# Kernel tuning notes

Measured on AMD Instinct MI355X. Metric: run time of the kernel, lower is better.

Reference implementation:

```python
import jax, jax.numpy as jnp
import numpy as np

P = 2  # sampling ratio: keep top ceil(M/p) measurements


def setup_inputs() -> dict:
    key = jax.random.key(0)
    k1, k2, k3 = jax.random.split(key, 3)
    B, H, W, C = 8, 1024, 1024, 3
    Y = jax.random.normal(k1, (B, H, W, C), dtype=jnp.float32)
    # build()-time Z0 components: abs ~ N(0.5, 0.1), angle ~ N(0, 0.5*sqrt(pi))
    Z0_abs = 0.5 + 0.1 * jax.random.normal(k2, (1, 1, H, W), dtype=jnp.float32)
    Z0_angle = (0.5 * np.pi ** 0.5) * jax.random.normal(k3, (1, 1, H, W), dtype=jnp.float32)
    return {"Y": Y, "Z0_abs": Z0_abs, "Z0_angle": Z0_angle}


def _make_Z0(Z0_abs, Z0_angle):
    # Z0 = |Z0| * exp(i*angle), Frobenius-normalized over spatial axes (2,3)
    Z0 = Z0_abs.astype(jnp.complex64) * jnp.exp(1j * Z0_angle.astype(jnp.complex64))
    fro = jnp.sqrt(jnp.sum(jnp.abs(Z0) ** 2, axis=(2, 3), keepdims=True)).astype(jnp.complex64)
    return Z0 / fro


def reference(Y, Z0_abs, Z0_angle):
    B, H, W, C = Y.shape
    M = H * W * C
    R = int(np.ceil(M / P))
    # transpose NHWC -> NCHW, scale by original S[2] (= W)
    Y_S = jnp.transpose(Y.astype(jnp.float32), (0, 3, 1, 2)) / jnp.float32(W)
    y_s = Y_S.reshape(B, M)
    # threshold = R-th largest value per batch (== descending-sorted index R-1)
    thr = jax.lax.top_k(y_s, R)[0][:, -1]  # [B]
    Ytr = (Y_S >= thr[:, None, None, None]).astype(jnp.float32)  # [B,C,H,W]
    Z0 = _make_Z0(Z0_abs, Z0_angle)
    return Ytr, Z0
```

## Files before the change

kernel.cpp:

```cpp
#include <hip/hip_runtime.h>
#include <math.h>

#define BATCH 8
#define HH 1024
#define WW 1024
#define CC 3
#define MTOT (HH*WW*CC)
#define RSEL 1572864u

#define WCAP 131072u
#define LCAP 1024u
#define P1B  2048
#define QPT  4

#define U_HI 0xBC800000u
#define U_LO 0x437FFFFFu

#define WS_WCNT_OFF  0u
#define WS_CHI_OFF   512u
#define WS_NPART_OFF 1024u
#define WS_THR_OFF   2048u
#define WS_FB_OFF    2112u
#define WS_WU_OFF    4096u
#define WS_WP_OFF    4198400u

#define NCOPY 3
#define HSTRIDE 4097

__device__ __forceinline__ unsigned int fmap(float x) {
    unsigned int b = __float_as_uint(x);
    return (b & 0x80000000u) ? ~b : (b | 0x80000000u);
}

__device__ __forceinline__ void thresh_row_quad(const float* __restrict__ Yb,
                                                float* __restrict__ outb,
                                                int h, int w4, unsigned int tu) {
    const float4* src = (const float4*)(Yb + ((size_t)h * WW + (size_t)w4 * 4) * CC);
    float4 a0 = src[0], a1 = src[1], a2 = src[2];
    float4 r0, r1, r2;
    r0.x = (fmap(a0.x) >= tu) ? 1.f : 0.f;
    r0.y = (fmap(a0.w) >= tu) ? 1.f : 0.f;
    r0.z = (fmap(a1.z) >= tu) ? 1.f : 0.f;
    r0.w = (fmap(a2.y) >= tu) ? 1.f : 0.f;
    r1.x = (fmap(a0.y) >= tu) ? 1.f : 0.f;
    r1.y = (fmap(a1.x) >= tu) ? 1.f : 0.f;
    r1.z = (fmap(a1.w) >= tu) ? 1.f : 0.f;
    r1.w = (fmap(a2.z) >= tu) ? 1.f : 0.f;
    r2.x = (fmap(a0.z) >= tu) ? 1.f : 0.f;
    r2.y = (fmap(a1.y) >= tu) ? 1.f : 0.f;
    r2.z = (fmap(a2.x) >= tu) ? 1.f : 0.f;
    r2.w = (fmap(a2.w) >= tu) ? 1.f : 0.f;
    size_t base = (size_t)h * WW;
    ((float4*)(outb + base))[w4]                        = r0;
    ((float4*)(outb + base + (size_t)HH * WW))[w4]      = r1;
    ((float4*)(outb + base + (size_t)2 * HH * WW))[w4]  = r2;
}

__global__ void __launch_bounds__(256, 4) pass1_kernel(
                             const float* __restrict__ Y,
                             const float* __restrict__ zabs,
                             float* __restrict__ out,
                             unsigned int* __restrict__ wu,
                             unsigned int* __restrict__ wpos,
                             unsigned int* __restrict__ wcnt,
                             unsigned int* __restrict__ chib,
                             float* __restrict__ npart) {
    const int tid = threadIdx.x;

    if (blockIdx.x >= P1B) {
        const int bx = blockIdx.x - P1B;
        float s = 0.f;
        const int n4z = HH * WW / 4;
        for (int i = bx * 256 + tid; i < n4z; i += 256 * 256) {
            float4 v = ((const float4*)zabs)[i];
            s += v.x * v.x + v.y * v.y + v.z * v.z + v.w * v.w;
        }
        for (int d = 32; d > 0; d >>= 1) s += __shfl_down(s, d);
        __shared__ float ls[4];
        if ((tid & 63) == 0) ls[tid >> 6] = s;
        __syncthreads();
        if (tid == 0) npart[bx] = ls[0] + ls[1] + ls[2] + ls[3];
        return;
    }

    __shared__ unsigned int lu[LCAP];
    __shared__ unsigned int lp[LCAP];
    __shared__ unsigned int lcnt;
    __shared__ unsigned int red[4];
    __shared__ unsigned int gbase_s;
    if (tid == 0) lcnt = 0u;
    __syncthreads();

    const int blk = blockIdx.x;
    const int b = blk >> 8;
    const int p0 = (blk & 255) * 1024 + tid;
    const float* Yb = Y + (size_t)b * MTOT;
    float* outb = out + (size_t)b * MTOT;
    float4* o4 = (float4*)outb;

    float4 A0[QPT], A1[QPT], A2[QPT];
#pragma unroll
    for (int it = 0; it < QPT; it++) {
        int p = p0 + it * 256;
        const float4* src = (const float4*)(Yb + (size_t)p * 12);
        A0[it] = src[0]; A1[it] = src[1]; A2[it] = src[2];
    }
    __builtin_amdgcn_sched_barrier(0);

    unsigned int hcnt = 0u;
    unsigned long long wmask = 0ull;

#pragma unroll
    for (int it = 0; it < QPT; it++) {
        const int p = p0 + it * 256;
        float4 a0 = A0[it], a1 = A1[it], a2 = A2[it];
        float4 r0, r1, r2;

#define CLS(val, dst, j) do { \
        unsigned int u = fmap(val); \
        bool hi = (u >= U_HI); \
        dst = hi ? 1.f : 0.f; \
        hcnt += hi ? 1u : 0u; \
        if (!hi && u >= U_LO) wmask |= (1ull << (it * 12 + (j))); \
    } while (0)

        CLS(a0.x, r0.x, 0); CLS(a0.w, r0.y, 1); CLS(a1.z, r0.z, 2); CLS(a2.y, r0.w, 3);
        CLS(a0.y, r1.x, 4); CLS(a1.x, r1.y, 5); CLS(a1.w, r1.z, 6); CLS(a2.z, r1.w, 7);
        CLS(a0.z, r2.x, 8); CLS(a1.y, r2.y, 9); CLS(a2.x, r2.z, 10); CLS(a2.w, r2.w, 11);
#undef CLS

        o4[p]           = r0;
        o4[262144 + p]  = r1;
        o4[524288 + p]  = r2;
    }

    if (wmask) {
        unsigned int nw = (unsigned int)__popcll(wmask);
        unsigned int base = atomicAdd(&lcnt, nw);
#pragma unroll
        for (int it = 0; it < QPT; it++) {
            const int p = p0 + it * 256;
            const unsigned int rb = (unsigned int)(4 * p);
            float4 a0 = A0[it], a1 = A1[it], a2 = A2[it];
#define EMIT(val, ch, k, j) do { \
            if (wmask & (1ull << (it * 12 + (j)))) { \
                if (base < LCAP) { lu[base] = fmap(val); lp[base] = (unsigned int)((ch) * HH * WW) + rb + (k); } \
                base++; \
            } \
        } while (0)
            EMIT(a0.x, 0, 0, 0); EMIT(a0.w, 0, 1, 1); EMIT(a1.z, 0, 2, 2); EMIT(a2.y, 0, 3, 3);
            EMIT(a0.y, 1, 0, 4); EMIT(a1.x, 1, 1, 5); EMIT(a1.w, 1, 2, 6); EMIT(a2.z, 1, 3, 7);
            EMIT(a0.z, 2, 0, 8); EMIT(a1.y, 2, 1, 9); EMIT(a2.x, 2, 2, 10); EMIT(a2.w, 2, 3, 11);
#undef EMIT
        }
    }

    __syncthreads();
    unsigned int n = lcnt;
    unsigned int nc = (n > LCAP) ? LCAP : n;
    if (tid == 0) {
        unsigned int add = (n > LCAP) ? (WCAP + 1u) : n;
        gbase_s = atomicAdd(&wcnt[b * 16], add);
    }
    for (int d = 32; d > 0; d >>= 1) hcnt += __shfl_down(hcnt, d);
    if ((tid & 63) == 0) red[tid >> 6] = hcnt;
    __syncthreads();
    if (tid == 0) atomicAdd(&chib[b * 16], red[0] + red[1] + red[2] + red[3]);

    unsigned int gbase = gbase_s;
    unsigned int* wub = wu + (size_t)b * WCAP;
    unsigned int* wpb = wpos + (size_t)b * WCAP;
    for (unsigned int j = tid; j < nc; j += 256u) {
        unsigned int q = gbase + j;
        if (q < WCAP) { wub[q] = lu[j]; wpb[q] = lp[j]; }
    }
}

__global__ void __launch_bounds__(1024) refine_kernel(
        const float* __restrict__ Y,
        const unsigned int* __restrict__ wu,
        const unsigned int* __restrict__ wcnt,
        const unsigned int* __restrict__ chib,
        const float* __restrict__ npart,
        unsigned int* __restrict__ thr,
        unsigned int* __restrict__ fbflag,
        const float* __restrict__ zabs,
        const float* __restrict__ zang,
        float* __restrict__ outz, int interleaved) {
    const int tid = threadIdx.x;

    if (blockIdx.x >= 8) {
        const int z = blockIdx.x - 8;
        __shared__ float ls[4];
        float s = (tid < 256) ? npart[tid] : 0.f;
        for (int d = 32; d > 0; d >>= 1) s += __shfl_down(s, d);
        if (tid < 256 && (tid & 63) == 0) ls[tid >> 6] = s;
        __syncthreads();
        float inv = 1.0f / sqrtf(ls[0] + ls[1] + ls[2] + ls[3]);
        int i = z * 1024 + tid;
        float2 a = ((const float2*)zabs)[i];
        float2 g = ((const float2*)zang)[i];
        float s0, c0, s1, c1;
        __sincosf(g.x, &s0, &c0);
        __sincosf(g.y, &s1, &c1);
        if (interleaved) {
            float4 o;
            o.x = a.x * c0 * inv; o.y = a.x * s0 * inv;
            o.z = a.y * c1 * inv; o.w = a.y * s1 * inv;
            ((float4*)outz)[i] = o;
        } else {
            float2 o;
            o.x = a.x * c0 * inv; o.y = a.y * c1 * inv;
            ((float2*)outz)[i] = o;
        }
        return;
    }

    __shared__ unsigned int hist[NCOPY * HSTRIDE];
    __shared__ unsigned int waveSums[16];
    __shared__ unsigned int selBin, selBase;
    const int b = blockIdx.x;
    const int lane = tid & 63, wid = tid >> 6;
    const int hc = (wid % NCOPY) * HSTRIDE;

    const unsigned int wc = wcnt[b * 16];
    const unsigned int Ch = chib[b * 16];
    const int fb = (wc > WCAP) || (Ch >= RSEL) || (Ch + wc < RSEL);
    unsigned int target = fb ? RSEL : (RSEL - Ch);
    const unsigned int wcg = (wc > WCAP) ? WCAP : wc;
    const unsigned int* wp = wu + (size_t)b * WCAP;
    const float* Yb = Y + (size_t)b * MTOT;

    unsigned int d1 = 0, d2 = 0;

    for (int level = 0; level < 3; level++) {
        const int nb  = (level < 2) ? 4096 : 256;
        const int bpt = (level < 2) ? 4 : 1;
        for (int i = tid; i < NCOPY * HSTRIDE; i += 1024) hist[i] = 0u;
        if (tid == 0) { selBin = 0u; selBase = 0u; }
        __syncthreads();

#define HISTO(u) do { \
            if (level == 0) atomicAdd(&hist[hc + ((u) >> 20)], 1u); \
            else if (level == 1) { if (((u) >> 20) == d1) atomicAdd(&hist[hc + (((u) >> 8) & 0xFFFu)], 1u); } \
            else { if (((u) >> 8) == ((d1 << 12) | d2)) atomicAdd(&hist[hc + ((u) & 0xFFu)], 1u); } \
        } while (0)

        if (fb) {
            for (unsigned int i = tid; i < (unsigned int)MTOT; i += 1024u) {
                unsigned int u = fmap(Yb[i]);
                HISTO(u);
            }
        } else {
            for (unsigned int i = tid; i < wcg; i += 1024u) {
                unsigned int u = wp[i];
                HISTO(u);
            }
        }
#undef HISTO
        __syncthreads();
        unsigned int c[4] = {0u, 0u, 0u, 0u};
        unsigned int s = 0u;
        const int nthr = nb / bpt;
        if (tid < nthr)
            for (int k = 0; k < bpt; k++) {
                int bin = nb - 1 - (tid * bpt + k);
                c[k] = hist[bin] + hist[HSTRIDE + bin] + hist[2 * HSTRIDE + bin];
                s += c[k];
            }
        unsigned int incl = s;
        for (int d = 1; d < 64; d <<= 1) {
            unsigned int v = __shfl_up(incl, d);
            if (lane >= d) incl += v;
        }
        if (lane == 63) waveSums[wid] = incl;
        __syncthreads();
        if (tid < 16) {
            unsigned int w = waveSums[tid];
            for (int d = 1; d < 16; d <<= 1) {
                unsigned int v = __shfl_up(w, d);
                if (tid >= d) w += v;
            }
            waveSums[tid] = w;
        }
        __syncthreads();
        incl += (wid > 0) ? waveSums[wid - 1] : 0u;
        unsigned int excl = incl - s;
        if (s > 0u && excl < target && incl >= target) {
            unsigned int run = excl;
            for (int k = 0; k < bpt; k++) {
                if (run + c[k] >= target) {
                    selBin = (unsigned int)(nb - 1 - (tid * bpt + k));
                    selBase = run;
                    break;
                }
                run += c[k];
            }
        }
        __syncthreads();
        if (level == 0) d1 = selBin;
        else if (level == 1) d2 = selBin;
        target -= selBase;
        __syncthreads();
    }
    if (tid == 0) {
        thr[b] = (d1 << 20) | (d2 << 8) | selBin;
        fbflag[b] = (unsigned int)fb;
    }
}

__global__ void fixup_kernel(const float* __restrict__ Y,
                             const unsigned int* __restrict__ wu,
                             const unsigned int* __restrict__ wpos,
                             const unsigned int* __restrict__ wcnt,
                             const unsigned int* __restrict__ thr,
                             const unsigned int* __restrict__ fbflag,
                             float* __restrict__ out) {
    const int tid = threadIdx.x;
    const int j = blockIdx.x;
    const int b = j >> 5;
    const unsigned int tu = thr[b];
    float* outb = out + (size_t)b * MTOT;
    if (fbflag[b]) {
        const float* Yb = Y + (size_t)b * MTOT;
        for (int q = (j & 31) * 256 + tid; q < 262144; q += 8192) {
            thresh_row_quad(Yb, outb, q >> 8, q & 255, tu);
        }
    } else {
        const unsigned int wc = wcnt[b * 16];
        const unsigned int* wub = wu + (size_t)b * WCAP;
        const unsigned int* wpb = wpos + (size_t)b * WCAP;
        for (unsigned int i = (unsigned int)(j & 31) * 256u + tid; i < wc; i += 8192u) {
            outb[wpb[i]] = (wub[i] >= tu) ? 1.f : 0.f;
        }
    }
}

extern "C" void kernel_launch(void* const* d_in, const int* in_sizes, int n_in,
                              void* d_out, int out_size, void* d_ws, size_t ws_size,
                              hipStream_t stream) {
    const float* Y    = (const float*)d_in[0];
    const float* zabs = (const float*)d_in[1];
    const float* zang = (const float*)d_in[2];
    float* out = (float*)d_out;

    unsigned char* ws = (unsigned char*)d_ws;
    unsigned int* wcnt  = (unsigned int*)(ws + WS_WCNT_OFF);
    unsigned int* chib  = (unsigned int*)(ws + WS_CHI_OFF);
    float*        npart = (float*)(ws + WS_NPART_OFF);
    unsigned int* thr   = (unsigned int*)(ws + WS_THR_OFF);
    unsigned int* fbf   = (unsigned int*)(ws + WS_FB_OFF);
    unsigned int* wu    = (unsigned int*)(ws + WS_WU_OFF);
    unsigned int* wpos  = (unsigned int*)(ws + WS_WP_OFF);

    (void)hipMemsetAsync(ws, 0, 1024, stream);

    pass1_kernel<<<P1B + 256, 256, 0, stream>>>(Y, zabs, out, wu, wpos, wcnt, chib, npart);

    size_t zoff = (size_t)BATCH * CC * HH * WW;
    int zfloats = out_size - (int)zoff;
    int interleaved = (zfloats >= 2 * HH * WW) ? 1 : 0;

    refine_kernel<<<8 + 512, 1024, 0, stream>>>(
        Y, wu, wcnt, chib, npart, thr, fbf, zabs, zang, out + zoff, interleaved);

    fixup_kernel<<<256, 256, 0, stream>>>(Y, wu, wpos, wcnt, thr, fbf, out);
}
```

Before: 244.6 us.

## Fuse fixup into refine kernel and double per-thread work in pass1

Folds the fixup scatter into the tail of refine_kernel, so each batch block applies its own threshold right after computing it. This removes one kernel launch and the threshold/fallback-flag round trip through global memory. Separately, pass1 now processes 8 quads per thread with half as many blocks and a lower occupancy hint, splitting the window mask into two 64-bit words. The cost is that the fixup (including the full-tensor fallback path) now runs on only 8 blocks instead of 256, which could serialize if the fallback triggers.

Measured after the change: 275.4 us. +12.6%, slower.

```diff
diff --git a/kernel.cpp b/kernel.cpp
--- a/kernel.cpp
+++ b/kernel.cpp
@@ -10,8 +10,8 @@
 
 #define WCAP 131072u
 #define LCAP 1024u
-#define P1B  2048
-#define QPT  4
+#define P1B  1024
+#define QPT  8
 
 #define U_HI 0xBC800000u
 #define U_LO 0x437FFFFFu
@@ -20,7 +20,6 @@
 #define WS_CHI_OFF   512u
 #define WS_NPART_OFF 1024u
 #define WS_THR_OFF   2048u
-#define WS_FB_OFF    2112u
 #define WS_WU_OFF    4096u
 #define WS_WP_OFF    4198400u
 
@@ -56,7 +55,7 @@
     ((float4*)(outb + base + (size_t)2 * HH * WW))[w4]  = r2;
 }
 
-__global__ void __launch_bounds__(256, 4) pass1_kernel(
+__global__ void __launch_bounds__(256, 3) pass1_kernel(
                              const float* __restrict__ Y,
                              const float* __restrict__ zabs,
                              float* __restrict__ out,
@@ -92,8 +91,8 @@
     __syncthreads();
 
     const int blk = blockIdx.x;
-    const int b = blk >> 8;
-    const int p0 = (blk & 255) * 1024 + tid;
+    const int b = blk >> 7;
+    const int p0 = (blk & 127) * 2048 + tid;
     const float* Yb = Y + (size_t)b * MTOT;
     float* outb = out + (size_t)b * MTOT;
     float4* o4 = (float4*)outb;
@@ -108,7 +107,7 @@
     __builtin_amdgcn_sched_barrier(0);
 
     unsigned int hcnt = 0u;
-    unsigned long long wmask = 0ull;
+    unsigned long long wm[2] = {0ull, 0ull};
 
 #pragma unroll
     for (int it = 0; it < QPT; it++) {
@@ -121,7 +120,7 @@
         bool hi = (u >= U_HI); \
         dst = hi ? 1.f : 0.f; \
         hcnt += hi ? 1u : 0u; \
-        if (!hi && u >= U_LO) wmask |= (1ull << (it * 12 + (j))); \
+        if (!hi && u >= U_LO) wm[it >> 2] |= (1ull << ((it & 3) * 12 + (j))); \
     } while (0)
 
         CLS(a0.x, r0.x, 0); CLS(a0.w, r0.y, 1); CLS(a1.z, r0.z, 2); CLS(a2.y, r0.w, 3);
@@ -134,8 +133,8 @@
         o4[524288 + p]  = r2;
     }
 
-    if (wmask) {
-        unsigned int nw = (unsigned int)__popcll(wmask);
+    if (wm[0] | wm[1]) {
+        unsigned int nw = (unsigned int)(__popcll(wm[0]) + __popcll(wm[1]));
         unsigned int base = atomicAdd(&lcnt, nw);
 #pragma unroll
         for (int it = 0; it < QPT; it++) {
@@ -143,7 +142,7 @@
             const unsigned int rb = (unsigned int)(4 * p);
             float4 a0 = A0[it], a1 = A1[it], a2 = A2[it];
 #define EMIT(val, ch, k, j) do { \
-            if (wmask & (1ull << (it * 12 + (j)))) { \
+            if (wm[it >> 2] & (1ull << ((it & 3) * 12 + (j)))) { \
                 if (base < LCAP) { lu[base] = fmap(val); lp[base] = (unsigned int)((ch) * HH * WW) + rb + (k); } \
                 base++; \
             } \
@@ -179,11 +178,12 @@
 __global__ void __launch_bounds__(1024) refine_kernel(
         const float* __restrict__ Y,
         const unsigned int* __restrict__ wu,
+        const unsigned int* __restrict__ wpos,
         const unsigned int* __restrict__ wcnt,
         const unsigned int* __restrict__ chib,
         const float* __restrict__ npart,
         unsigned int* __restrict__ thr,
-        unsigned int* __restrict__ fbflag,
+        float* __restrict__ out,
         const float* __restrict__ zabs,
         const float* __restrict__ zang,
         float* __restrict__ outz, int interleaved) {
@@ -219,6 +219,7 @@
     __shared__ unsigned int hist[NCOPY * HSTRIDE];
     __shared__ unsigned int waveSums[16];
     __shared__ unsigned int selBin, selBase;
+    __shared__ unsigned int thr_s;
     const int b = blockIdx.x;
     const int lane = tid & 63, wid = tid >> 6;
     const int hc = (wid % NCOPY) * HSTRIDE;
@@ -304,35 +305,20 @@
         __syncthreads();
     }
     if (tid == 0) {
-        thr[b] = (d1 << 20) | (d2 << 8) | selBin;
-        fbflag[b] = (unsigned int)fb;
-    }
-}
-
-__global__ void fixup_kernel(const float* __restrict__ Y,
-                             const unsigned int* __restrict__ wu,
-                             const unsigned int* __restrict__ wpos,
-                             const unsigned int* __restrict__ wcnt,
-                             const unsigned int* __restrict__ thr,
-                             const unsigned int* __restrict__ fbflag,
-                             float* __restrict__ out) {
-    const int tid = threadIdx.x;
-    const int j = blockIdx.x;
-    const int b = j >> 5;
-    const unsigned int tu = thr[b];
+        thr_s = (d1 << 20) | (d2 << 8) | selBin;
+        thr[b] = thr_s;
+    }
+    __syncthreads();
+
+    const unsigned int tu = thr_s;
     float* outb = out + (size_t)b * MTOT;
-    if (fbflag[b]) {
-        const float* Yb = Y + (size_t)b * MTOT;
-        for (int q = (j & 31) * 256 + tid; q < 262144; q += 8192) {
+    if (fb) {
+        for (int q = tid; q < 262144; q += 1024)
             thresh_row_quad(Yb, outb, q >> 8, q & 255, tu);
-        }
     } else {
-        const unsigned int wc = wcnt[b * 16];
-        const unsigned int* wub = wu + (size_t)b * WCAP;
         const unsigned int* wpb = wpos + (size_t)b * WCAP;
-        for (unsigned int i = (unsigned int)(j & 31) * 256u + tid; i < wc; i += 8192u) {
-            outb[wpb[i]] = (wub[i] >= tu) ? 1.f : 0.f;
-        }
+        for (unsigned int i = tid; i < wc; i += 1024u)
+            outb[wpb[i]] = (wp[i] >= tu) ? 1.f : 0.f;
     }
 }
 
@@ -349,7 +335,6 @@
     unsigned int* chib  = (unsigned int*)(ws + WS_CHI_OFF);
     float*        npart = (float*)(ws + WS_NPART_OFF);
     unsigned int* thr   = (unsigned int*)(ws + WS_THR_OFF);
-    unsigned int* fbf   = (unsigned int*)(ws + WS_FB_OFF);
     unsigned int* wu    = (unsigned int*)(ws + WS_WU_OFF);
     unsigned int* wpos  = (unsigned int*)(ws + WS_WP_OFF);
 
@@ -362,7 +347,5 @@
     int interleaved = (zfloats >= 2 * HH * WW) ? 1 : 0;
 
     refine_kernel<<<8 + 512, 1024, 0, stream>>>(
-        Y, wu, wcnt, chib, npart, thr, fbf, zabs, zang, out + zoff, interleaved);
-
-    fixup_kernel<<<256, 256, 0, stream>>>(Y, wu, wpos, wcnt, thr, fbf, out);
-}
+        Y, wu, wpos, wcnt, chib, npart, thr, out, zabs, zang, out + zoff, interleaved);
+}
```
